# Kernel tuning notes

Measured on AMD Instinct MI355X. Metric: run time of the kernel, lower is better.

## Reference

```python
import jax, jax.numpy as jnp
import numpy as np

D = 256          # input_dim (node embedding dim)
ATT_TIMES = 2
ATT_NUM = 2
DIN = D * ATT_NUM  # NTN input dim = 512
F = 16           # feature_map_dim


def setup_inputs() -> dict:
    key = jax.random.key(0)
    ks = jax.random.split(key, 10)
    x1 = jax.random.normal(ks[0], (120000, D), dtype=jnp.float32)
    x2 = jax.random.normal(ks[1], (100000, D), dtype=jnp.float32)
    # attention weight (glorot)
    W0 = jax.random.normal(ks[2], (D, D), dtype=jnp.float32) * (2.0 / (D + D)) ** 0.5
    # NTN params
    V = jax.random.normal(ks[3], (F, 2 * DIN), dtype=jnp.float32) * (2.0 / (F + 2 * DIN)) ** 0.5
    W = jax.random.normal(ks[4], (F, DIN, DIN), dtype=jnp.float32) * (2.0 / (DIN + DIN)) ** 0.5
    b = jax.random.normal(ks[5], (F,), dtype=jnp.float32)
    # projection MLP 16->8->4->2->1, torch Linear weights are (out, in)
    P0 = jax.random.normal(ks[6], (8, 16), dtype=jnp.float32) * (2.0 / (8 + 16)) ** 0.5
    P1 = jax.random.normal(ks[7], (4, 8), dtype=jnp.float32) * (2.0 / (4 + 8)) ** 0.5
    P2 = jax.random.normal(ks[8], (2, 4), dtype=jnp.float32) * (2.0 / (2 + 4)) ** 0.5
    P3 = jax.random.normal(ks[9], (1, 2), dtype=jnp.float32) * (2.0 / (1 + 2)) ** 0.5
    return {"x1": x1, "x2": x2, "W0": W0, "V": V, "W": W, "b": b,
            "P0": P0, "P1": P1, "P2": P2, "P3": P3}


def _attention(x, W0):
    # x: (N, D) -> (1, D*ATT_NUM) graph embedding.
    outs = []
    for _ in range(ATT_NUM):  # 'dot' style: same params each head (eye W), kept for faithfulness
        cur = x
        out = None
        for _ in range(ATT_TIMES):
            temp = jnp.mean(cur, axis=0, keepdims=True)          # (1, D)
            h_avg = jnp.tanh(temp @ W0)                          # att_weight=True
            att = jax.nn.sigmoid(cur @ h_avg.T)                  # (N, 1), W=eye in 'dot' style
            out = att.T @ cur                                    # (1, D)
            cur = cur * att
        outs.append(out)
    return jnp.concatenate(outs, axis=1)                         # (1, DIN)


def _ntn(g1, g2, V, W, b):
    # g1, g2: (1, DIN). Fused bilinear over all F feature maps.
    concat = jnp.concatenate([g1, g2], axis=1)                   # (1, 2*DIN)
    v_term = concat @ V.T                                        # (1, F)
    w_term = jnp.einsum('nd,fde,me->nf', g1, W, g2)              # (1, F)
    return jax.nn.sigmoid(v_term + w_term + b)                   # inneract = sigmoid


def reference(x1, x2, W0, V, W, b, P0, P1, P2, P3):
    g1 = _attention(x1, W0)
    g2 = _attention(x2, W0)
    x = _ntn(g1, g2, V, W, b)                                    # (1, F), branch 'an'
    for P in (P0, P1, P2, P3):                                   # Linear(no bias) + Sigmoid
        x = jax.nn.sigmoid(x @ P.T)
    return x                                                     # (1, 1)
```

## Files before the change

### kernel.cpp

```cpp
#include <hip/hip_runtime.h>
#include <math.h>

#define DD 256
#define REPS 8

#define OFF_SUMREP 0
#define OFF_H1     4096
#define OFF_S1REP  4608
#define OFF_H2     8704
#define OFF_OREP   9216
#define OFF_O      13312
#define OFF_WTREP  13824
#define WS_FLOATS  13952

__device__ __forceinline__ float sigmoidf_(float x) { return 1.0f / (1.0f + __expf(-x)); }

__device__ __forceinline__ float wave_sum(float v) {
#pragma unroll
    for (int off = 32; off; off >>= 1) v += __shfl_xor(v, off, 64);
    return v;
}

__global__ void k_zero(float* __restrict__ ws) {
    int i = blockIdx.x * 256 + threadIdx.x;
    if (i < WS_FLOATS) ws[i] = 0.0f;
}

__global__ void k_mean(const float* __restrict__ x1, const float* __restrict__ x2,
                       int N1, int N2, float* __restrict__ ws) {
    int b = blockIdx.x, t = threadIdx.x;
    int inp = (b < 512) ? 0 : 1;
    int bl = inp ? (b - 512) : b;
    const float4* x = (const float4*)(inp ? x2 : x1);
    int N = inp ? N2 : N1;
    int col4 = t & 63;
    int rg = t >> 6;
    float4 acc = make_float4(0.f, 0.f, 0.f, 0.f);
    for (int r = bl * 4 + rg; r < N; r += 2048) {
        float4 v = x[(size_t)r * 64 + col4];
        acc.x += v.x; acc.y += v.y; acc.z += v.z; acc.w += v.w;
    }
    __shared__ float4 lds[256];
    lds[t] = acc;
    __syncthreads();
    if (t < 64) {
        float4 s = lds[t];
        float4 a = lds[t + 64], c = lds[t + 128], d = lds[t + 192];
        s.x += a.x + c.x + d.x; s.y += a.y + c.y + d.y;
        s.z += a.z + c.z + d.z; s.w += a.w + c.w + d.w;
        float* dst = ws + OFF_SUMREP + inp * (REPS * 256) + (bl & (REPS - 1)) * 256 + t * 4;
        atomicAdd(dst + 0, s.x); atomicAdd(dst + 1, s.y);
        atomicAdd(dst + 2, s.z); atomicAdd(dst + 3, s.w);
    }
}

__global__ void k_h(const float* __restrict__ W0, float* __restrict__ ws,
                    int srcOff, int dstOff, int N1, int N2) {
    int inp = blockIdx.x, t = threadIdx.x;
    __shared__ float temp[256];
    const float* src = ws + srcOff + inp * (REPS * 256);
    float s = 0.f;
#pragma unroll
    for (int r = 0; r < REPS; r++) s += src[r * 256 + t];
    temp[t] = s * (1.0f / (float)(inp ? N2 : N1));
    __syncthreads();
    float h0 = 0.f, h1 = 0.f, h2 = 0.f, h3 = 0.f;
#pragma unroll 4
    for (int d = 0; d < 256; d += 4) {
        h0 += temp[d + 0] * W0[(d + 0) * 256 + t];
        h1 += temp[d + 1] * W0[(d + 1) * 256 + t];
        h2 += temp[d + 2] * W0[(d + 2) * 256 + t];
        h3 += temp[d + 3] * W0[(d + 3) * 256 + t];
    }
    ws[dstOff + inp * 256 + t] = tanhf((h0 + h1) + (h2 + h3));
}

__global__ void k_att1(const float* __restrict__ x1, const float* __restrict__ x2,
                       int N1, int N2, float* __restrict__ ws) {
    int b = blockIdx.x, t = threadIdx.x;
    int inp = (b < 512) ? 0 : 1;
    int bl = inp ? (b - 512) : b;
    const float4* x = (const float4*)(inp ? x2 : x1);
    int N = inp ? N2 : N1;
    int lane = t & 63, w = t >> 6;
    float4 h1 = ((const float4*)(ws + OFF_H1 + inp * 256))[lane];
    float4 acc = make_float4(0.f, 0.f, 0.f, 0.f);
    for (int r = bl * 4 + w; r < N; r += 2048) {
        float4 v = x[(size_t)r * 64 + lane];
        float d = v.x * h1.x + v.y * h1.y + v.z * h1.z + v.w * h1.w;
        d = wave_sum(d);
        float att = sigmoidf_(d);
        acc.x += att * v.x; acc.y += att * v.y; acc.z += att * v.z; acc.w += att * v.w;
    }
    __shared__ float4 lds[256];
    lds[t] = acc;
    __syncthreads();
    if (t < 64) {
        float4 s = lds[t];
        float4 a = lds[t + 64], c = lds[t + 128], d = lds[t + 192];
        s.x += a.x + c.x + d.x; s.y += a.y + c.y + d.y;
        s.z += a.z + c.z + d.z; s.w += a.w + c.w + d.w;
        float* dst = ws + OFF_S1REP + inp * (REPS * 256) + (bl & (REPS - 1)) * 256 + t * 4;
        atomicAdd(dst + 0, s.x); atomicAdd(dst + 1, s.y);
        atomicAdd(dst + 2, s.z); atomicAdd(dst + 3, s.w);
    }
}

__global__ void k_att2(const float* __restrict__ x1, const float* __restrict__ x2,
                       int N1, int N2, float* __restrict__ ws) {
    int b = blockIdx.x, t = threadIdx.x;
    int inp = (b < 512) ? 0 : 1;
    int bl = inp ? (b - 512) : b;
    const float4* x = (const float4*)(inp ? x2 : x1);
    int N = inp ? N2 : N1;
    int lane = t & 63, w = t >> 6;
    float4 h1 = ((const float4*)(ws + OFF_H1 + inp * 256))[lane];
    float4 h2 = ((const float4*)(ws + OFF_H2 + inp * 256))[lane];
    float4 acc = make_float4(0.f, 0.f, 0.f, 0.f);
    for (int r = bl * 4 + w; r < N; r += 2048) {
        float4 v = x[(size_t)r * 64 + lane];
        float d1 = v.x * h1.x + v.y * h1.y + v.z * h1.z + v.w * h1.w;
        float d2 = v.x * h2.x + v.y * h2.y + v.z * h2.z + v.w * h2.w;
#pragma unroll
        for (int off = 32; off; off >>= 1) {
            d1 += __shfl_xor(d1, off, 64);
            d2 += __shfl_xor(d2, off, 64);
        }
        float att1 = sigmoidf_(d1);
        float att2 = sigmoidf_(att1 * d2);
        float wgt = att1 * att2;
        acc.x += wgt * v.x; acc.y += wgt * v.y; acc.z += wgt * v.z; acc.w += wgt * v.w;
    }
    __shared__ float4 lds[256];
    lds[t] = acc;
    __syncthreads();
    if (t < 64) {
        float4 s = lds[t];
        float4 a = lds[t + 64], c = lds[t + 128], d = lds[t + 192];
        s.x += a.x + c.x + d.x; s.y += a.y + c.y + d.y;
        s.z += a.z + c.z + d.z; s.w += a.w + c.w + d.w;
        float* dst = ws + OFF_OREP + inp * (REPS * 256) + (bl & (REPS - 1)) * 256 + t * 4;
        atomicAdd(dst + 0, s.x); atomicAdd(dst + 1, s.y);
        atomicAdd(dst + 2, s.z); atomicAdd(dst + 3, s.w);
    }
}

__global__ void k_comb(float* __restrict__ ws) {
    int t = threadIdx.x;
    int inp = t >> 8, c = t & 255;
    float s = 0.f;
#pragma unroll
    for (int r = 0; r < REPS; r++) s += ws[OFF_OREP + inp * (REPS * 256) + r * 256 + c];
    ws[OFF_O + t] = s;
}

__global__ void k_ntn(const float* __restrict__ W, float* __restrict__ ws) {
    int b = blockIdx.x, t = threadIdx.x;
    int lane = t & 63, w = t >> 6;
    const float* o1 = ws + OFF_O;
    float4 o2f = ((const float4*)(ws + OFF_O + 256))[lane];
    for (int row = b * 4 + w; row < 8192; row += 2048) {
        int f = row >> 9, d = row & 511;
        const float4* Wr = (const float4*)(W + (size_t)row * 512);
        float4 a = Wr[lane];
        float4 c = Wr[lane + 64];
        float p = (a.x + c.x) * o2f.x + (a.y + c.y) * o2f.y
                + (a.z + c.z) * o2f.z + (a.w + c.w) * o2f.w;
        p = wave_sum(p);
        if (lane == 0)
            atomicAdd(ws + OFF_WTREP + (b & (REPS - 1)) * 16 + f, o1[d & 255] * p);
    }
}

__global__ void k_final(const float* __restrict__ V, const float* __restrict__ bb,
                        const float* __restrict__ P0, const float* __restrict__ P1,
                        const float* __restrict__ P2, const float* __restrict__ P3,
                        float* __restrict__ ws, float* __restrict__ out) {
    int t = threadIdx.x;
    const float* o = ws + OFF_O;
    int f = t >> 4, j = t & 15;
    float p = 0.f;
    for (int k = j; k < 1024; k += 16) {
        float cv = (k < 512) ? o[k & 255] : o[256 + (k & 255)];
        p += cv * V[f * 1024 + k];
    }
    __shared__ float red[256];
    __shared__ float sv[16];
    red[t] = p;
    __syncthreads();
    if (t < 16) {
        float v = 0.f;
#pragma unroll
        for (int q = 0; q < 16; q++) v += red[t * 16 + q];
        float wt = 0.f;
#pragma unroll
        for (int r = 0; r < REPS; r++) wt += ws[OFF_WTREP + r * 16 + t];
        sv[t] = sigmoidf_(v + wt + bb[t]);
    }
    __syncthreads();
    if (t == 0) {
        float y0[8], y1[4], y2[2];
#pragma unroll
        for (int i = 0; i < 8; i++) {
            float s = 0.f;
            for (int k = 0; k < 16; k++) s += P0[i * 16 + k] * sv[k];
            y0[i] = sigmoidf_(s);
        }
#pragma unroll
        for (int i = 0; i < 4; i++) {
            float s = 0.f;
            for (int k = 0; k < 8; k++) s += P1[i * 8 + k] * y0[k];
            y1[i] = sigmoidf_(s);
        }
#pragma unroll
        for (int i = 0; i < 2; i++) {
            float s = 0.f;
            for (int k = 0; k < 4; k++) s += P2[i * 4 + k] * y1[k];
            y2[i] = sigmoidf_(s);
        }
        out[0] = sigmoidf_(P3[0] * y2[0] + P3[1] * y2[1]);
    }
}

extern "C" void kernel_launch(void* const* d_in, const int* in_sizes, int n_in,
                              void* d_out, int out_size, void* d_ws, size_t ws_size,
                              hipStream_t stream) {
    const float* x1 = (const float*)d_in[0];
    const float* x2 = (const float*)d_in[1];
    const float* W0 = (const float*)d_in[2];
    const float* V  = (const float*)d_in[3];
    const float* W  = (const float*)d_in[4];
    const float* b  = (const float*)d_in[5];
    const float* P0 = (const float*)d_in[6];
    const float* P1 = (const float*)d_in[7];
    const float* P2 = (const float*)d_in[8];
    const float* P3 = (const float*)d_in[9];
    float* ws  = (float*)d_ws;
    float* out = (float*)d_out;
    int N1 = in_sizes[0] / DD;
    int N2 = in_sizes[1] / DD;

    k_zero <<<55,   256, 0, stream>>>(ws);
    k_mean <<<1024, 256, 0, stream>>>(x1, x2, N1, N2, ws);
    k_h    <<<2,    256, 0, stream>>>(W0, ws, OFF_SUMREP, OFF_H1, N1, N2);
    k_att1 <<<1024, 256, 0, stream>>>(x1, x2, N1, N2, ws);
    k_h    <<<2,    256, 0, stream>>>(W0, ws, OFF_S1REP, OFF_H2, N1, N2);
    k_att2 <<<1024, 256, 0, stream>>>(x1, x2, N1, N2, ws);
    k_comb <<<1,    512, 0, stream>>>(ws);
    k_ntn  <<<512,  256, 0, stream>>>(W, ws);
    k_final<<<1,    256, 0, stream>>>(V, b, P0, P1, P2, P3, ws, out);
}
```

Before: 427.3 us.

## Use contiguous row chunks, 4-row unrolled loads, split h-projection, and unroll NTN rows

The streaming kernels now give each block a contiguous chunk of rows instead of a grid-stride over rows, double the grid to 2048 blocks, and load four rows per iteration so more memory requests are in flight. The h projection is split across 32 blocks that atomically accumulate pre-activations, with tanh applied later inside the attention kernels. The NTN kernel processes four rows per wave with a single atomic. This adds more atomics and changes the floating-point summation order.

```diff
diff --git a/kernel.cpp b/kernel.cpp
--- a/kernel.cpp
+++ b/kernel.cpp
@@ -5,16 +5,21 @@
 #define REPS 8
 
 #define OFF_SUMREP 0
-#define OFF_H1     4096
+#define OFF_H1P    4096
 #define OFF_S1REP  4608
-#define OFF_H2     8704
+#define OFF_H2P    8704
 #define OFF_OREP   9216
 #define OFF_O      13312
 #define OFF_WTREP  13824
 #define WS_FLOATS  13952
 
 __device__ __forceinline__ float sigmoidf_(float x) { return 1.0f / (1.0f + __expf(-x)); }
-
+__device__ __forceinline__ float dot4(float4 a, float4 b) {
+    return a.x * b.x + a.y * b.y + a.z * b.z + a.w * b.w;
+}
+__device__ __forceinline__ void fma4(float4& acc, float s, float4 v) {
+    acc.x += s * v.x; acc.y += s * v.y; acc.z += s * v.z; acc.w += s * v.w;
+}
 __device__ __forceinline__ float wave_sum(float v) {
 #pragma unroll
     for (int off = 32; off; off >>= 1) v += __shfl_xor(v, off, 64);
@@ -26,20 +31,7 @@
     if (i < WS_FLOATS) ws[i] = 0.0f;
 }
 
-__global__ void k_mean(const float* __restrict__ x1, const float* __restrict__ x2,
-                       int N1, int N2, float* __restrict__ ws) {
-    int b = blockIdx.x, t = threadIdx.x;
-    int inp = (b < 512) ? 0 : 1;
-    int bl = inp ? (b - 512) : b;
-    const float4* x = (const float4*)(inp ? x2 : x1);
-    int N = inp ? N2 : N1;
-    int col4 = t & 63;
-    int rg = t >> 6;
-    float4 acc = make_float4(0.f, 0.f, 0.f, 0.f);
-    for (int r = bl * 4 + rg; r < N; r += 2048) {
-        float4 v = x[(size_t)r * 64 + col4];
-        acc.x += v.x; acc.y += v.y; acc.z += v.z; acc.w += v.w;
-    }
+__device__ __forceinline__ void block_reduce_atomic(float4 acc, int t, float* dst_base) {
     __shared__ float4 lds[256];
     lds[t] = acc;
     __syncthreads();
@@ -48,101 +40,142 @@
         float4 a = lds[t + 64], c = lds[t + 128], d = lds[t + 192];
         s.x += a.x + c.x + d.x; s.y += a.y + c.y + d.y;
         s.z += a.z + c.z + d.z; s.w += a.w + c.w + d.w;
-        float* dst = ws + OFF_SUMREP + inp * (REPS * 256) + (bl & (REPS - 1)) * 256 + t * 4;
+        float* dst = dst_base + t * 4;
         atomicAdd(dst + 0, s.x); atomicAdd(dst + 1, s.y);
         atomicAdd(dst + 2, s.z); atomicAdd(dst + 3, s.w);
     }
 }
 
-__global__ void k_h(const float* __restrict__ W0, float* __restrict__ ws,
-                    int srcOff, int dstOff, int N1, int N2) {
-    int inp = blockIdx.x, t = threadIdx.x;
-    __shared__ float temp[256];
-    const float* src = ws + srcOff + inp * (REPS * 256);
-    float s = 0.f;
-#pragma unroll
-    for (int r = 0; r < REPS; r++) s += src[r * 256 + t];
-    temp[t] = s * (1.0f / (float)(inp ? N2 : N1));
-    __syncthreads();
-    float h0 = 0.f, h1 = 0.f, h2 = 0.f, h3 = 0.f;
-#pragma unroll 4
-    for (int d = 0; d < 256; d += 4) {
-        h0 += temp[d + 0] * W0[(d + 0) * 256 + t];
-        h1 += temp[d + 1] * W0[(d + 1) * 256 + t];
-        h2 += temp[d + 2] * W0[(d + 2) * 256 + t];
-        h3 += temp[d + 3] * W0[(d + 3) * 256 + t];
-    }
-    ws[dstOff + inp * 256 + t] = tanhf((h0 + h1) + (h2 + h3));
-}
-
-__global__ void k_att1(const float* __restrict__ x1, const float* __restrict__ x2,
-                       int N1, int N2, float* __restrict__ ws) {
+__global__ void __launch_bounds__(256, 8)
+k_mean(const float* __restrict__ x1, const float* __restrict__ x2,
+       int N1, int N2, float* __restrict__ ws) {
     int b = blockIdx.x, t = threadIdx.x;
-    int inp = (b < 512) ? 0 : 1;
-    int bl = inp ? (b - 512) : b;
+    int inp = b >> 10;
+    int bl = b & 1023;
     const float4* x = (const float4*)(inp ? x2 : x1);
     int N = inp ? N2 : N1;
+    int chunk = (N + 1023) >> 10;
+    int start = bl * chunk;
+    int end = min(start + chunk, N);
     int lane = t & 63, w = t >> 6;
-    float4 h1 = ((const float4*)(ws + OFF_H1 + inp * 256))[lane];
-    float4 acc = make_float4(0.f, 0.f, 0.f, 0.f);
-    for (int r = bl * 4 + w; r < N; r += 2048) {
+    float4 a0 = make_float4(0.f, 0.f, 0.f, 0.f), a1 = a0;
+    int r = start + w;
+    for (; r + 12 < end; r += 16) {
+        const float4* p = x + (size_t)r * 64 + lane;
+        float4 v0 = p[0], v1 = p[256], v2 = p[512], v3 = p[768];
+        a0.x += v0.x + v1.x; a0.y += v0.y + v1.y; a0.z += v0.z + v1.z; a0.w += v0.w + v1.w;
+        a1.x += v2.x + v3.x; a1.y += v2.y + v3.y; a1.z += v2.z + v3.z; a1.w += v2.w + v3.w;
+    }
+    for (; r < end; r += 4) {
         float4 v = x[(size_t)r * 64 + lane];
-        float d = v.x * h1.x + v.y * h1.y + v.z * h1.z + v.w * h1.w;
-        d = wave_sum(d);
-        float att = sigmoidf_(d);
-        acc.x += att * v.x; acc.y += att * v.y; acc.z += att * v.z; acc.w += att * v.w;
-    }
-    __shared__ float4 lds[256];
-    lds[t] = acc;
+        a0.x += v.x; a0.y += v.y; a0.z += v.z; a0.w += v.w;
+    }
+    a0.x += a1.x; a0.y += a1.y; a0.z += a1.z; a0.w += a1.w;
+    block_reduce_atomic(a0, t, ws + OFF_SUMREP + inp * (REPS * 256) + (bl & (REPS - 1)) * 256);
+}
+
+__global__ void k_hpart(const float* __restrict__ W0, float* __restrict__ ws,
+                        int srcOff, int dstOff, int N1, int N2) {
+    int inp = blockIdx.x >> 4, g = blockIdx.x & 15;
+    int t = threadIdx.x;
+    __shared__ float temp[16];
+    if (t < 16) {
+        const float* src = ws + srcOff + inp * (REPS * 256) + g * 16 + t;
+        float s = 0.f;
+#pragma unroll
+        for (int r = 0; r < REPS; r++) s += src[r * 256];
+        temp[t] = s * (1.0f / (float)(inp ? N2 : N1));
+    }
     __syncthreads();
-    if (t < 64) {
-        float4 s = lds[t];
-        float4 a = lds[t + 64], c = lds[t + 128], d = lds[t + 192];
-        s.x += a.x + c.x + d.x; s.y += a.y + c.y + d.y;
-        s.z += a.z + c.z + d.z; s.w += a.w + c.w + d.w;
-        float* dst = ws + OFF_S1REP + inp * (REPS * 256) + (bl & (REPS - 1)) * 256 + t * 4;
-        atomicAdd(dst + 0, s.x); atomicAdd(dst + 1, s.y);
-        atomicAdd(dst + 2, s.z); atomicAdd(dst + 3, s.w);
-    }
-}
-
-__global__ void k_att2(const float* __restrict__ x1, const float* __restrict__ x2,
-                       int N1, int N2, float* __restrict__ ws) {
+    float p = 0.f;
+#pragma unroll
+    for (int j = 0; j < 16; j++) p += temp[j] * W0[(g * 16 + j) * 256 + t];
+    atomicAdd(ws + dstOff + inp * 256 + t, p);
+}
+
+__global__ void __launch_bounds__(256, 8)
+k_att1(const float* __restrict__ x1, const float* __restrict__ x2,
+       int N1, int N2, float* __restrict__ ws) {
     int b = blockIdx.x, t = threadIdx.x;
-    int inp = (b < 512) ? 0 : 1;
-    int bl = inp ? (b - 512) : b;
+    int inp = b >> 10;
+    int bl = b & 1023;
     const float4* x = (const float4*)(inp ? x2 : x1);
     int N = inp ? N2 : N1;
+    int chunk = (N + 1023) >> 10;
+    int start = bl * chunk;
+    int end = min(start + chunk, N);
     int lane = t & 63, w = t >> 6;
-    float4 h1 = ((const float4*)(ws + OFF_H1 + inp * 256))[lane];
-    float4 h2 = ((const float4*)(ws + OFF_H2 + inp * 256))[lane];
+    float4 hp = ((const float4*)(ws + OFF_H1P + inp * 256))[lane];
+    float4 h1 = make_float4(tanhf(hp.x), tanhf(hp.y), tanhf(hp.z), tanhf(hp.w));
     float4 acc = make_float4(0.f, 0.f, 0.f, 0.f);
-    for (int r = bl * 4 + w; r < N; r += 2048) {
+    int r = start + w;
+    for (; r + 12 < end; r += 16) {
+        const float4* p = x + (size_t)r * 64 + lane;
+        float4 v0 = p[0], v1 = p[256], v2 = p[512], v3 = p[768];
+        float d0 = dot4(v0, h1), d1 = dot4(v1, h1), d2 = dot4(v2, h1), d3 = dot4(v3, h1);
+#pragma unroll
+        for (int off = 32; off; off >>= 1) {
+            d0 += __shfl_xor(d0, off, 64); d1 += __shfl_xor(d1, off, 64);
+            d2 += __shfl_xor(d2, off, 64); d3 += __shfl_xor(d3, off, 64);
+        }
+        fma4(acc, sigmoidf_(d0), v0); fma4(acc, sigmoidf_(d1), v1);
+        fma4(acc, sigmoidf_(d2), v2); fma4(acc, sigmoidf_(d3), v3);
+    }
+    for (; r < end; r += 4) {
         float4 v = x[(size_t)r * 64 + lane];
-        float d1 = v.x * h1.x + v.y * h1.y + v.z * h1.z + v.w * h1.w;
-        float d2 = v.x * h2.x + v.y * h2.y + v.z * h2.z + v.w * h2.w;
+        float d = wave_sum(dot4(v, h1));
+        fma4(acc, sigmoidf_(d), v);
+    }
+    block_reduce_atomic(acc, t, ws + OFF_S1REP + inp * (REPS * 256) + (bl & (REPS - 1)) * 256);
+}
+
+__global__ void __launch_bounds__(256, 8)
+k_att2(const float* __restrict__ x1, const float* __restrict__ x2,
+       int N1, int N2, float* __restrict__ ws) {
+    int b = blockIdx.x, t = threadIdx.x;
+    int inp = b >> 10;
+    int bl = b & 1023;
+    const float4* x = (const float4*)(inp ? x2 : x1);
+    int N = inp ? N2 : N1;
+    int chunk = (N + 1023) >> 10;
+    int start = bl * chunk;
+    int end = min(start + chunk, N);
+    int lane = t & 63, w = t >> 6;
+    float4 hp1 = ((const float4*)(ws + OFF_H1P + inp * 256))[lane];
+    float4 hp2 = ((const float4*)(ws + OFF_H2P + inp * 256))[lane];
+    float4 h1 = make_float4(tanhf(hp1.x), tanhf(hp1.y), tanhf(hp1.z), tanhf(hp1.w));
+    float4 h2 = make_float4(tanhf(hp2.x), tanhf(hp2.y), tanhf(hp2.z), tanhf(hp2.w));
+    float4 acc = make_float4(0.f, 0.f, 0.f, 0.f);
+    int r = start + w;
+    for (; r + 12 < end; r += 16) {
+        const float4* p = x + (size_t)r * 64 + lane;
+        float4 v0 = p[0], v1 = p[256], v2 = p[512], v3 = p[768];
+        float d0 = dot4(v0, h1), d1 = dot4(v1, h1), d2 = dot4(v2, h1), d3 = dot4(v3, h1);
+        float e0 = dot4(v0, h2), e1 = dot4(v1, h2), e2 = dot4(v2, h2), e3 = dot4(v3, h2);
 #pragma unroll
         for (int off = 32; off; off >>= 1) {
-            d1 += __shfl_xor(d1, off, 64);
-            d2 += __shfl_xor(d2, off, 64);
-        }
-        float att1 = sigmoidf_(d1);
-        float att2 = sigmoidf_(att1 * d2);
-        float wgt = att1 * att2;
-        acc.x += wgt * v.x; acc.y += wgt * v.y; acc.z += wgt * v.z; acc.w += wgt * v.w;
-    }
-    __shared__ float4 lds[256];
-    lds[t] = acc;
-    __syncthreads();
-    if (t < 64) {
-        float4 s = lds[t];
-        float4 a = lds[t + 64], c = lds[t + 128], d = lds[t + 192];
-        s.x += a.x + c.x + d.x; s.y += a.y + c.y + d.y;
-        s.z += a.z + c.z + d.z; s.w += a.w + c.w + d.w;
-        float* dst = ws + OFF_OREP + inp * (REPS * 256) + (bl & (REPS - 1)) * 256 + t * 4;
-        atomicAdd(dst + 0, s.x); atomicAdd(dst + 1, s.y);
-        atomicAdd(dst + 2, s.z); atomicAdd(dst + 3, s.w);
-    }
+            d0 += __shfl_xor(d0, off, 64); e0 += __shfl_xor(e0, off, 64);
+            d1 += __shfl_xor(d1, off, 64); e1 += __shfl_xor(e1, off, 64);
+            d2 += __shfl_xor(d2, off, 64); e2 += __shfl_xor(e2, off, 64);
+            d3 += __shfl_xor(d3, off, 64); e3 += __shfl_xor(e3, off, 64);
+        }
+        float a1_0 = sigmoidf_(d0), a1_1 = sigmoidf_(d1), a1_2 = sigmoidf_(d2), a1_3 = sigmoidf_(d3);
+        fma4(acc, a1_0 * sigmoidf_(a1_0 * e0), v0);
+        fma4(acc, a1_1 * sigmoidf_(a1_1 * e1), v1);
+        fma4(acc, a1_2 * sigmoidf_(a1_2 * e2), v2);
+        fma4(acc, a1_3 * sigmoidf_(a1_3 * e3), v3);
+    }
+    for (; r < end; r += 4) {
+        float4 v = x[(size_t)r * 64 + lane];
+        float d = dot4(v, h1), e = dot4(v, h2);
+#pragma unroll
+        for (int off = 32; off; off >>= 1) {
+            d += __shfl_xor(d, off, 64); e += __shfl_xor(e, off, 64);
+        }
+        float a1 = sigmoidf_(d);
+        fma4(acc, a1 * sigmoidf_(a1 * e), v);
+    }
+    block_reduce_atomic(acc, t, ws + OFF_OREP + inp * (REPS * 256) + (bl & (REPS - 1)) * 256);
 }
 
 __global__ void k_comb(float* __restrict__ ws) {
@@ -154,21 +187,39 @@
     ws[OFF_O + t] = s;
 }
 
-__global__ void k_ntn(const float* __restrict__ W, float* __restrict__ ws) {
+__global__ void __launch_bounds__(256, 8)
+k_ntn(const float* __restrict__ W, float* __restrict__ ws) {
     int b = blockIdx.x, t = threadIdx.x;
     int lane = t & 63, w = t >> 6;
     const float* o1 = ws + OFF_O;
     float4 o2f = ((const float4*)(ws + OFF_O + 256))[lane];
-    for (int row = b * 4 + w; row < 8192; row += 2048) {
-        int f = row >> 9, d = row & 511;
-        const float4* Wr = (const float4*)(W + (size_t)row * 512);
-        float4 a = Wr[lane];
-        float4 c = Wr[lane + 64];
-        float p = (a.x + c.x) * o2f.x + (a.y + c.y) * o2f.y
-                + (a.z + c.z) * o2f.z + (a.w + c.w) * o2f.w;
-        p = wave_sum(p);
-        if (lane == 0)
-            atomicAdd(ws + OFF_WTREP + (b & (REPS - 1)) * 16 + f, o1[d & 255] * p);
+    int f = b >> 5;
+    int r0 = b * 16 + w;
+    const float4* W4 = (const float4*)W;
+    float p0, p1, p2, p3;
+    {
+        const float4* q0 = W4 + (size_t)r0 * 128 + lane;
+        float4 a0 = q0[0],   c0 = q0[64];
+        float4 a1 = q0[512], c1 = q0[576];
+        float4 a2 = q0[1024], c2 = q0[1088];
+        float4 a3 = q0[1536], c3 = q0[1600];
+        p0 = (a0.x + c0.x) * o2f.x + (a0.y + c0.y) * o2f.y + (a0.z + c0.z) * o2f.z + (a0.w + c0.w) * o2f.w;
+        p1 = (a1.x + c1.x) * o2f.x + (a1.y + c1.y) * o2f.y + (a1.z + c1.z) * o2f.z + (a1.w + c1.w) * o2f.w;
+        p2 = (a2.x + c2.x) * o2f.x + (a2.y + c2.y) * o2f.y + (a2.z + c2.z) * o2f.z + (a2.w + c2.w) * o2f.w;
+        p3 = (a3.x + c3.x) * o2f.x + (a3.y + c3.y) * o2f.y + (a3.z + c3.z) * o2f.z + (a3.w + c3.w) * o2f.w;
+    }
+#pragma unroll
+    for (int off = 32; off; off >>= 1) {
+        p0 += __shfl_xor(p0, off, 64); p1 += __shfl_xor(p1, off, 64);
+        p2 += __shfl_xor(p2, off, 64); p3 += __shfl_xor(p3, off, 64);
+    }
+    if (lane == 0) {
+        float* dst = ws + OFF_WTREP + (b & (REPS - 1)) * 16 + f;
+        int d = r0 & 511;
+        atomicAdd(dst, o1[d & 255] * p0
+                     + o1[(d + 4) & 255] * p1
+                     + o1[(d + 8) & 255] * p2
+                     + o1[(d + 12) & 255] * p3);
     }
 }
 
@@ -240,13 +291,13 @@
     int N1 = in_sizes[0] / DD;
     int N2 = in_sizes[1] / DD;
 
-    k_zero <<<55,   256, 0, stream>>>(ws);
-    k_mean <<<1024, 256, 0, stream>>>(x1, x2, N1, N2, ws);
-    k_h    <<<2,    256, 0, stream>>>(W0, ws, OFF_SUMREP, OFF_H1, N1, N2);
-    k_att1 <<<1024, 256, 0, stream>>>(x1, x2, N1, N2, ws);
-    k_h    <<<2,    256, 0, stream>>>(W0, ws, OFF_S1REP, OFF_H2, N1, N2);
-    k_att2 <<<1024, 256, 0, stream>>>(x1, x2, N1, N2, ws);
-    k_comb <<<1,    512, 0, stream>>>(ws);
-    k_ntn  <<<512,  256, 0, stream>>>(W, ws);
-    k_final<<<1,    256, 0, stream>>>(V, b, P0, P1, P2, P3, ws, out);
-}
+    k_zero  <<<55,   256, 0, stream>>>(ws);
+    k_mean  <<<2048, 256, 0, stream>>>(x1, x2, N1, N2, ws);
+    k_hpart <<<32,   256, 0, stream>>>(W0, ws, OFF_SUMREP, OFF_H1P, N1, N2);
+    k_att1  <<<2048, 256, 0, stream>>>(x1, x2, N1, N2, ws);
+    k_hpart <<<32,   256, 0, stream>>>(W0, ws, OFF_S1REP, OFF_H2P, N1, N2);
+    k_att2  <<<2048, 256, 0, stream>>>(x1, x2, N1, N2, ws);
+    k_comb  <<<1,    512, 0, stream>>>(ws);
+    k_ntn   <<<512,  256, 0, stream>>>(W, ws);
+    k_final <<<1,    256, 0, stream>>>(V, b, P0, P1, P2, P3, ws, out);
+}
```

Result: faster. 418.7 us (-2.0%).
